# Kernel optimization log

Hardware: AMD Instinct MI355X
Metric: run time of the kernel (lower is better)

Reference implementation:

```python
import jax, jax.numpy as jnp
import numpy as np

N_NODES = 50000
N_EDGES = 300000
D_IN = 256
D_HID = 256


def setup_inputs() -> dict:
    key = jax.random.key(0)
    ks = jax.random.split(key, 9)
    x = jax.random.normal(ks[0], (N_NODES, D_IN), dtype=jnp.float32)
    src = jax.random.randint(ks[1], (N_EDGES,), 0, N_NODES, dtype=jnp.int64)
    dst = jax.random.randint(ks[2], (N_EDGES,), 0, N_NODES, dtype=jnp.int64)
    # Kaiming-uniform-ish init like nn.Linear defaults
    def lin(k, fan_in, fan_out):
        bound = 1.0 / np.sqrt(fan_in)
        kw, kb = jax.random.split(k)
        W = jax.random.uniform(kw, (fan_out, fan_in), minval=-bound, maxval=bound, dtype=jnp.float32)
        b = jax.random.uniform(kb, (fan_out,), minval=-bound, maxval=bound, dtype=jnp.float32)
        return W, b
    W1, b1 = lin(ks[3], 2 * D_IN, D_HID)
    W2, b2 = lin(ks[4], D_HID, D_HID)
    W3, b3 = lin(ks[5], D_HID, 1)
    return {"x": x, "src": src, "dst": dst,
            "W1": W1, "b1": b1, "W2": W2, "b2": b2, "W3": W3, "b3": b3}


def reference(x, src, dst, W1, b1, W2, b2, W3, b3):
    # gather src/dst node features per edge and concat -> [E, 2*D_IN]
    h = jnp.concatenate([x[src], x[dst]], axis=1)
    h = jax.nn.relu(h @ W1.T + b1)          # [E, D_HID]
    h = jax.nn.relu(h @ W2.T + b2)          # dropout is identity in eval mode
    score = h @ W3.T + b3                   # [E, 1]
    return score
```

## Files before the change

kernel.cpp:

```cpp
#include <hip/hip_runtime.h>

typedef short bfx8 __attribute__((ext_vector_type(8)));
typedef short bfx4 __attribute__((ext_vector_type(4)));
typedef float fx4 __attribute__((ext_vector_type(4)));

#define E_TILE 64

__device__ __forceinline__ short f2b(float f) {
  union { float f; unsigned u; } v; v.f = f;
  unsigned u = v.u;
  u += 0x7fffu + ((u >> 16) & 1u);
  return (short)(u >> 16);
}
__device__ __forceinline__ float relu(float f) { return f > 0.f ? f : 0.f; }
__device__ __forceinline__ float asf(unsigned u) { union { unsigned u; float f; } v; v.u = u; return v.f; }
__device__ __forceinline__ unsigned asu(float f) { union { float f; unsigned u; } v; v.f = f; return v.u; }

__global__ void k_prep(const float* __restrict__ W1, const float* __restrict__ W2,
                       unsigned short* __restrict__ B1, unsigned short* __restrict__ W2b) {
  int t = blockIdx.x * 256 + threadIdx.x;
  if (t < 512 * 256) {
    int n = t >> 8, k = t & 255;
    float v = (n < 256) ? W1[n * 512 + k] : W1[(n - 256) * 512 + 256 + k];
    B1[t] = (unsigned short)f2b(v);
  } else if (t < 512 * 256 + 256 * 256) {
    int i = t - 512 * 256;
    W2b[i] = (unsigned short)f2b(W2[i]);
  }
}

__launch_bounds__(512, 4)
__global__ void k_node(const float* __restrict__ x, const unsigned short* __restrict__ B1,
                       const float* __restrict__ b1,
                       unsigned short* __restrict__ PQ, int n_nodes) {
  __shared__ __align__(16) short smA[64 * 40];
  __shared__ __align__(16) short smW[512 * 40];
  short* smT = smW;
  const int tid = threadIdx.x;
  const int wave = tid >> 6, lane = tid & 63;
  const int lr = lane & 15, lg = lane >> 4;
  const int m0 = blockIdx.x * 64;

  fx4 acc[4][4] = {};

#pragma unroll 1
  for (int ks = 0; ks < 8; ++ks) {
    const int k0 = ks * 32;
    {
      int r = tid >> 3, c = (tid & 7) * 4;
      int m = m0 + r;
      bfx4 o;
      if (m < n_nodes) {
        float4 v = *(const float4*)(x + (size_t)m * 256 + k0 + c);
        o[0] = f2b(v.x); o[1] = f2b(v.y); o[2] = f2b(v.z); o[3] = f2b(v.w);
      } else {
        o = (bfx4){0, 0, 0, 0};
      }
      *(bfx4*)&smA[r * 40 + c] = o;
    }
#pragma unroll
    for (int it = 0; it < 4; ++it) {
      int idx = it * 512 + tid;
      int n = idx >> 2, c = (idx & 3) * 8;
      *(bfx8*)&smW[n * 40 + c] = *(const bfx8*)(B1 + n * 256 + k0 + c);
    }
    __syncthreads();
    bfx8 af[4];
#pragma unroll
    for (int mt = 0; mt < 4; ++mt)
      af[mt] = *(const bfx8*)&smA[(mt * 16 + lr) * 40 + lg * 8];
#pragma unroll
    for (int nt = 0; nt < 4; ++nt) {
      bfx8 bf = *(const bfx8*)&smW[(wave * 64 + nt * 16 + lr) * 40 + lg * 8];
#pragma unroll
      for (int mt = 0; mt < 4; ++mt)
        acc[mt][nt] = __builtin_amdgcn_mfma_f32_16x16x32_bf16(af[mt], bf, acc[mt][nt], 0, 0, 0);
    }
    __syncthreads();
  }

  float bias[4];
#pragma unroll
  for (int nt = 0; nt < 4; ++nt) {
    int n = wave * 64 + nt * 16 + lr;
    bias[nt] = (n >= 256) ? b1[n - 256] : 0.f;
  }

#pragma unroll
  for (int h = 0; h < 2; ++h) {
#pragma unroll
    for (int mt2 = 0; mt2 < 2; ++mt2) {
      const int mt = 2 * h + mt2;
#pragma unroll
      for (int nt = 0; nt < 4; ++nt)
#pragma unroll
        for (int i = 0; i < 4; ++i) {
          int mrow = mt2 * 16 + lg * 4 + i;
          int n = wave * 64 + nt * 16 + lr;
          smT[mrow * 520 + n] = f2b(acc[mt][nt][i] + bias[nt]);
        }
    }
    __syncthreads();
    int r = tid >> 4, cbase = (tid & 15) * 8;
    int m = m0 + h * 32 + r;
    if (m < n_nodes) {
#pragma unroll
      for (int j = 0; j < 4; ++j) {
        int c = cbase + j * 128;
        *(bfx8*)(PQ + (size_t)m * 512 + c) = *(const bfx8*)&smT[r * 520 + c];
      }
    }
    __syncthreads();
  }
}

__launch_bounds__(512, 4)
__global__ void k_edge(const unsigned short* __restrict__ PQ,
                       const int* __restrict__ src, const int* __restrict__ dst,
                       const unsigned short* __restrict__ W2b,
                       const float* __restrict__ b2, const float* __restrict__ W3,
                       const float* __restrict__ b3, float* __restrict__ out,
                       int E, int ntiles) {
  __shared__ __align__(16) short smH[64 * 264];
  __shared__ float smS[8][64];
  const int tid = threadIdx.x;
  const int wave = tid >> 6, lane = tid & 63;
  const int lr = lane & 15, lg = lane >> 4;

  bfx8 bw[2][8];
  float b2v[2], w3v[2];
#pragma unroll
  for (int nt = 0; nt < 2; ++nt) {
    int n = wave * 32 + nt * 16 + lr;
    b2v[nt] = b2[n];
    w3v[nt] = W3[n];
#pragma unroll
    for (int ks = 0; ks < 8; ++ks)
      bw[nt][ks] = *(const bfx8*)(W2b + n * 256 + ks * 32 + lg * 8);
  }
  const float b3v = b3[0];

  const int r = tid >> 3;
  const int stride = gridDim.x * E_TILE;

  int e0 = blockIdx.x * E_TILE + r;
  int s_cur = 0, d_cur = 0;
  if (e0 < E) { s_cur = src[e0]; d_cur = dst[e0]; }

  for (int tile = blockIdx.x; tile < ntiles; tile += gridDim.x) {
    const int base = tile * E_TILE;
    const int e = base + r;
    if (e < E) {
      const unsigned* ps = (const unsigned*)(PQ + (size_t)s_cur * 512);
      const unsigned* pd = (const unsigned*)(PQ + (size_t)d_cur * 512 + 256);
#pragma unroll
      for (int it = 0; it < 4; ++it) {
        int c = (tid & 7) * 8 + it * 64;
        uint4 pv = *(const uint4*)(ps + (c >> 1));
        uint4 qv = *(const uint4*)(pd + (c >> 1));
        unsigned o[4];
        const unsigned* pw = (const unsigned*)&pv;
        const unsigned* qw = (const unsigned*)&qv;
#pragma unroll
        for (int w = 0; w < 4; ++w) {
          unsigned up = pw[w], uq = qw[w];
          float slo = relu(asf(up << 16) + asf(uq << 16));
          float shi = relu(asf(up & 0xffff0000u) + asf(uq & 0xffff0000u));
          o[w] = __builtin_amdgcn_perm(asu(shi) + 0x8000u, asu(slo) + 0x8000u,
                                       0x07060302u);
        }
        *(uint4*)&smH[r * 264 + c] = make_uint4(o[0], o[1], o[2], o[3]);
      }
    } else {
#pragma unroll
      for (int it = 0; it < 4; ++it) {
        int c = (tid & 7) * 8 + it * 64;
        *(uint4*)&smH[r * 264 + c] = make_uint4(0, 0, 0, 0);
      }
    }
    int e_next = e + stride;
    if (e_next < E) { s_cur = src[e_next]; d_cur = dst[e_next]; }
    __syncthreads();

    fx4 acc[4][2] = {};
#pragma unroll
    for (int ks = 0; ks < 8; ++ks) {
      bfx8 af[4];
#pragma unroll
      for (int mt = 0; mt < 4; ++mt)
        af[mt] = *(const bfx8*)&smH[(mt * 16 + lr) * 264 + ks * 32 + lg * 8];
#pragma unroll
      for (int nt = 0; nt < 2; ++nt)
#pragma unroll
        for (int mt = 0; mt < 4; ++mt)
          acc[mt][nt] = __builtin_amdgcn_mfma_f32_16x16x32_bf16(af[mt], bw[nt][ks], acc[mt][nt], 0, 0, 0);
    }

#pragma unroll
    for (int mt = 0; mt < 4; ++mt)
#pragma unroll
      for (int i = 0; i < 4; ++i) {
        float p = 0.f;
#pragma unroll
        for (int nt = 0; nt < 2; ++nt)
          p += relu(acc[mt][nt][i] + b2v[nt]) * w3v[nt];
        p += __shfl_xor(p, 1);
        p += __shfl_xor(p, 2);
        p += __shfl_xor(p, 4);
        p += __shfl_xor(p, 8);
        if (lr == 0) smS[wave][mt * 16 + lg * 4 + i] = p;
      }
    __syncthreads();
    if (tid < 64) {
      int eo = base + tid;
      if (eo < E)
        out[eo] = smS[0][tid] + smS[1][tid] + smS[2][tid] + smS[3][tid] +
                  smS[4][tid] + smS[5][tid] + smS[6][tid] + smS[7][tid] + b3v;
    }
    __syncthreads();
  }
}

__global__ void k_fallback(const float* __restrict__ x, const int* __restrict__ src,
                           const int* __restrict__ dst, const float* __restrict__ W1,
                           const float* __restrict__ b1, const float* __restrict__ W2,
                           const float* __restrict__ b2, const float* __restrict__ W3,
                           const float* __restrict__ b3, float* __restrict__ out, int E) {
  __shared__ float smF[4][512];
  __shared__ float smG[4][256];
  int wave = threadIdx.x >> 6, lane = threadIdx.x & 63;
  int e = blockIdx.x * 4 + wave;
  bool valid = e < E;
  int ec = valid ? e : 0;
  int s = src[ec], d = dst[ec];
  for (int j = 0; j < 8; ++j) {
    int k = lane * 8 + j;
    smF[wave][k] = (k < 256) ? x[(size_t)s * 256 + k] : x[(size_t)d * 256 + k - 256];
  }
  __syncthreads();
  for (int t = 0; t < 4; ++t) {
    int n = lane + t * 64;
    float a = b1[n];
    for (int k = 0; k < 512; ++k) a += smF[wave][k] * W1[n * 512 + k];
    smG[wave][n] = relu(a);
  }
  __syncthreads();
  float p = 0.f;
  for (int t = 0; t < 4; ++t) {
    int n = lane + t * 64;
    float a = b2[n];
    for (int k = 0; k < 256; ++k) a += smG[wave][k] * W2[n * 256 + k];
    p += relu(a) * W3[n];
  }
  for (int m = 1; m < 64; m <<= 1) p += __shfl_xor(p, m);
  if (lane == 0 && valid) out[e] = p + b3[0];
}

extern "C" void kernel_launch(void* const* d_in, const int* in_sizes, int n_in,
                              void* d_out, int out_size, void* d_ws, size_t ws_size,
                              hipStream_t stream) {
  const float* x  = (const float*)d_in[0];
  const int*   src = (const int*)d_in[1];
  const int*   dst = (const int*)d_in[2];
  const float* W1 = (const float*)d_in[3];
  const float* b1 = (const float*)d_in[4];
  const float* W2 = (const float*)d_in[5];
  const float* b2 = (const float*)d_in[6];
  const float* W3 = (const float*)d_in[7];
  const float* b3 = (const float*)d_in[8];
  float* out = (float*)d_out;

  const int E = in_sizes[1];
  const int n_nodes = in_sizes[0] / 256;

  const size_t offB1 = 0;
  const size_t offW2 = (size_t)512 * 256 * 2;
  const size_t offPQ = offW2 + (size_t)256 * 256 * 2;
  const size_t need = offPQ + (size_t)n_nodes * 512 * 2;

  if (ws_size >= need) {
    unsigned short* B1  = (unsigned short*)((char*)d_ws + offB1);
    unsigned short* W2b = (unsigned short*)((char*)d_ws + offW2);
    unsigned short* PQ  = (unsigned short*)((char*)d_ws + offPQ);
    k_prep<<<768, 256, 0, stream>>>(W1, W2, B1, W2b);
    k_node<<<(n_nodes + 63) / 64, 512, 0, stream>>>(x, B1, b1, PQ, n_nodes);
    const int ntiles = (E + E_TILE - 1) / E_TILE;
    int grid = ntiles < 512 ? ntiles : 512;
    k_edge<<<grid, 512, 0, stream>>>(PQ, src, dst, W2b, b2, W3, b3, out, E, ntiles);
  } else {
    k_fallback<<<(E + 3) / 4, 256, 0, stream>>>(x, src, dst, W1, b1, W2, b2, W3, b3, out, E);
  }
}
```

Measured before the change: 235.6 us.

## Drop LDS staging in node GEMM, pre-convert x to bf16, widen edge blocks

A new pass converts x to bf16 ahead of time. The node GEMM then loads MFMA operands straight from global memory, which removes the shared-memory staging and its barriers inside the k-loop. The edge kernel moves to 1024-thread blocks of 128 edges, with each wave owning 16 output columns, and launches a grid of 256 blocks. The extra conversion pass costs additional global traffic and a launch. Uncoalesced direct global loads and lower occupancy at 1024 threads could offset the savings.

```diff
diff --git a/kernel.cpp b/kernel.cpp
--- a/kernel.cpp
+++ b/kernel.cpp
@@ -1,10 +1,9 @@
 #include <hip/hip_runtime.h>
 
 typedef short bfx8 __attribute__((ext_vector_type(8)));
-typedef short bfx4 __attribute__((ext_vector_type(4)));
 typedef float fx4 __attribute__((ext_vector_type(4)));
 
-#define E_TILE 64
+#define E_TILE 128
 
 __device__ __forceinline__ short f2b(float f) {
   union { float f; unsigned u; } v; v.f = f;
@@ -29,60 +28,70 @@
   }
 }
 
+__global__ __launch_bounds__(256) void k_convert(const float* __restrict__ x,
+                                                 unsigned short* __restrict__ xb, int n) {
+  int i = (blockIdx.x * 256 + threadIdx.x) * 8;
+  if (i < n) {
+    float4 a = *(const float4*)(x + i);
+    float4 b = *(const float4*)(x + i + 4);
+    bfx8 o;
+    o[0] = f2b(a.x); o[1] = f2b(a.y); o[2] = f2b(a.z); o[3] = f2b(a.w);
+    o[4] = f2b(b.x); o[5] = f2b(b.y); o[6] = f2b(b.z); o[7] = f2b(b.w);
+    *(bfx8*)(xb + i) = o;
+  }
+}
+
+template <bool USE_XB>
 __launch_bounds__(512, 4)
-__global__ void k_node(const float* __restrict__ x, const unsigned short* __restrict__ B1,
-                       const float* __restrict__ b1,
+__global__ void k_node(const float* __restrict__ x, const unsigned short* __restrict__ xb,
+                       const unsigned short* __restrict__ B1, const float* __restrict__ b1,
                        unsigned short* __restrict__ PQ, int n_nodes) {
-  __shared__ __align__(16) short smA[64 * 40];
-  __shared__ __align__(16) short smW[512 * 40];
-  short* smT = smW;
+  __shared__ __align__(16) short smT[32 * 520];
   const int tid = threadIdx.x;
   const int wave = tid >> 6, lane = tid & 63;
   const int lr = lane & 15, lg = lane >> 4;
   const int m0 = blockIdx.x * 64;
+  const int n0 = wave * 64;
+
+  int mrow[4];
+#pragma unroll
+  for (int mt = 0; mt < 4; ++mt) {
+    int m = m0 + mt * 16 + lr;
+    mrow[mt] = m < n_nodes ? m : (n_nodes - 1);
+  }
 
   fx4 acc[4][4] = {};
 
-#pragma unroll 1
+#pragma unroll 2
   for (int ks = 0; ks < 8; ++ks) {
-    const int k0 = ks * 32;
-    {
-      int r = tid >> 3, c = (tid & 7) * 4;
-      int m = m0 + r;
-      bfx4 o;
-      if (m < n_nodes) {
-        float4 v = *(const float4*)(x + (size_t)m * 256 + k0 + c);
-        o[0] = f2b(v.x); o[1] = f2b(v.y); o[2] = f2b(v.z); o[3] = f2b(v.w);
+    bfx8 af[4];
+#pragma unroll
+    for (int mt = 0; mt < 4; ++mt) {
+      if (USE_XB) {
+        af[mt] = *(const bfx8*)(xb + (size_t)mrow[mt] * 256 + ks * 32 + lg * 8);
       } else {
-        o = (bfx4){0, 0, 0, 0};
-      }
-      *(bfx4*)&smA[r * 40 + c] = o;
-    }
-#pragma unroll
-    for (int it = 0; it < 4; ++it) {
-      int idx = it * 512 + tid;
-      int n = idx >> 2, c = (idx & 3) * 8;
-      *(bfx8*)&smW[n * 40 + c] = *(const bfx8*)(B1 + n * 256 + k0 + c);
-    }
-    __syncthreads();
-    bfx8 af[4];
-#pragma unroll
-    for (int mt = 0; mt < 4; ++mt)
-      af[mt] = *(const bfx8*)&smA[(mt * 16 + lr) * 40 + lg * 8];
+        const float* p = x + (size_t)mrow[mt] * 256 + ks * 32 + lg * 8;
+        float4 v0 = *(const float4*)(p);
+        float4 v1 = *(const float4*)(p + 4);
+        bfx8 o;
+        o[0] = f2b(v0.x); o[1] = f2b(v0.y); o[2] = f2b(v0.z); o[3] = f2b(v0.w);
+        o[4] = f2b(v1.x); o[5] = f2b(v1.y); o[6] = f2b(v1.z); o[7] = f2b(v1.w);
+        af[mt] = o;
+      }
+    }
 #pragma unroll
     for (int nt = 0; nt < 4; ++nt) {
-      bfx8 bf = *(const bfx8*)&smW[(wave * 64 + nt * 16 + lr) * 40 + lg * 8];
+      bfx8 bf = *(const bfx8*)(B1 + (size_t)(n0 + nt * 16 + lr) * 256 + ks * 32 + lg * 8);
 #pragma unroll
       for (int mt = 0; mt < 4; ++mt)
         acc[mt][nt] = __builtin_amdgcn_mfma_f32_16x16x32_bf16(af[mt], bf, acc[mt][nt], 0, 0, 0);
     }
-    __syncthreads();
   }
 
   float bias[4];
 #pragma unroll
   for (int nt = 0; nt < 4; ++nt) {
-    int n = wave * 64 + nt * 16 + lr;
+    int n = n0 + nt * 16 + lr;
     bias[nt] = (n >= 256) ? b1[n - 256] : 0.f;
   }
 
@@ -95,9 +104,9 @@
       for (int nt = 0; nt < 4; ++nt)
 #pragma unroll
         for (int i = 0; i < 4; ++i) {
-          int mrow = mt2 * 16 + lg * 4 + i;
-          int n = wave * 64 + nt * 16 + lr;
-          smT[mrow * 520 + n] = f2b(acc[mt][nt][i] + bias[nt]);
+          int mr = mt2 * 16 + lg * 4 + i;
+          int n = n0 + nt * 16 + lr;
+          smT[mr * 520 + n] = f2b(acc[mt][nt][i] + bias[nt]);
         }
     }
     __syncthreads();
@@ -114,33 +123,33 @@
   }
 }
 
-__launch_bounds__(512, 4)
+__launch_bounds__(1024, 4)
 __global__ void k_edge(const unsigned short* __restrict__ PQ,
                        const int* __restrict__ src, const int* __restrict__ dst,
                        const unsigned short* __restrict__ W2b,
                        const float* __restrict__ b2, const float* __restrict__ W3,
                        const float* __restrict__ b3, float* __restrict__ out,
                        int E, int ntiles) {
-  __shared__ __align__(16) short smH[64 * 264];
-  __shared__ float smS[8][64];
+  __shared__ __align__(16) short smH[E_TILE * 264];
+  __shared__ float smS[16][E_TILE];
   const int tid = threadIdx.x;
   const int wave = tid >> 6, lane = tid & 63;
   const int lr = lane & 15, lg = lane >> 4;
 
-  bfx8 bw[2][8];
-  float b2v[2], w3v[2];
-#pragma unroll
-  for (int nt = 0; nt < 2; ++nt) {
-    int n = wave * 32 + nt * 16 + lr;
-    b2v[nt] = b2[n];
-    w3v[nt] = W3[n];
+  bfx8 bw[8];
+  float b2v, w3v;
+  {
+    int n = wave * 16 + lr;
+    b2v = b2[n];
+    w3v = W3[n];
 #pragma unroll
     for (int ks = 0; ks < 8; ++ks)
-      bw[nt][ks] = *(const bfx8*)(W2b + n * 256 + ks * 32 + lg * 8);
+      bw[ks] = *(const bfx8*)(W2b + (size_t)n * 256 + ks * 32 + lg * 8);
   }
   const float b3v = b3[0];
 
   const int r = tid >> 3;
+  const int sub = tid & 7;
   const int stride = gridDim.x * E_TILE;
 
   int e0 = blockIdx.x * E_TILE + r;
@@ -155,7 +164,7 @@
       const unsigned* pd = (const unsigned*)(PQ + (size_t)d_cur * 512 + 256);
 #pragma unroll
       for (int it = 0; it < 4; ++it) {
-        int c = (tid & 7) * 8 + it * 64;
+        int c = sub * 8 + it * 64;
         uint4 pv = *(const uint4*)(ps + (c >> 1));
         uint4 qv = *(const uint4*)(pd + (c >> 1));
         unsigned o[4];
@@ -174,7 +183,7 @@
     } else {
 #pragma unroll
       for (int it = 0; it < 4; ++it) {
-        int c = (tid & 7) * 8 + it * 64;
+        int c = sub * 8 + it * 64;
         *(uint4*)&smH[r * 264 + c] = make_uint4(0, 0, 0, 0);
       }
     }
@@ -182,28 +191,23 @@
     if (e_next < E) { s_cur = src[e_next]; d_cur = dst[e_next]; }
     __syncthreads();
 
-    fx4 acc[4][2] = {};
-#pragma unroll
+    fx4 acc[8];
+#pragma unroll
+    for (int mt = 0; mt < 8; ++mt) acc[mt] = (fx4){0.f, 0.f, 0.f, 0.f};
+#pragma unroll 1
     for (int ks = 0; ks < 8; ++ks) {
-      bfx8 af[4];
-#pragma unroll
-      for (int mt = 0; mt < 4; ++mt)
-        af[mt] = *(const bfx8*)&smH[(mt * 16 + lr) * 264 + ks * 32 + lg * 8];
-#pragma unroll
-      for (int nt = 0; nt < 2; ++nt)
-#pragma unroll
-        for (int mt = 0; mt < 4; ++mt)
-          acc[mt][nt] = __builtin_amdgcn_mfma_f32_16x16x32_bf16(af[mt], bw[nt][ks], acc[mt][nt], 0, 0, 0);
-    }
-
-#pragma unroll
-    for (int mt = 0; mt < 4; ++mt)
+#pragma unroll
+      for (int mt = 0; mt < 8; ++mt) {
+        bfx8 af = *(const bfx8*)&smH[(mt * 16 + lr) * 264 + ks * 32 + lg * 8];
+        acc[mt] = __builtin_amdgcn_mfma_f32_16x16x32_bf16(af, bw[ks], acc[mt], 0, 0, 0);
+      }
+    }
+
+#pragma unroll
+    for (int mt = 0; mt < 8; ++mt)
 #pragma unroll
       for (int i = 0; i < 4; ++i) {
-        float p = 0.f;
-#pragma unroll
-        for (int nt = 0; nt < 2; ++nt)
-          p += relu(acc[mt][nt][i] + b2v[nt]) * w3v[nt];
+        float p = relu(acc[mt][i] + b2v) * w3v;
         p += __shfl_xor(p, 1);
         p += __shfl_xor(p, 2);
         p += __shfl_xor(p, 4);
@@ -211,11 +215,14 @@
         if (lr == 0) smS[wave][mt * 16 + lg * 4 + i] = p;
       }
     __syncthreads();
-    if (tid < 64) {
+    if (tid < E_TILE) {
       int eo = base + tid;
-      if (eo < E)
-        out[eo] = smS[0][tid] + smS[1][tid] + smS[2][tid] + smS[3][tid] +
-                  smS[4][tid] + smS[5][tid] + smS[6][tid] + smS[7][tid] + b3v;
+      if (eo < E) {
+        float s = b3v;
+#pragma unroll
+        for (int w = 0; w < 16; ++w) s += smS[w][tid];
+        out[eo] = s;
+      }
     }
     __syncthreads();
   }
@@ -272,21 +279,35 @@
 
   const int E = in_sizes[1];
   const int n_nodes = in_sizes[0] / 256;
+  const int n_x = in_sizes[0];
 
   const size_t offB1 = 0;
   const size_t offW2 = (size_t)512 * 256 * 2;
-  const size_t offPQ = offW2 + (size_t)256 * 256 * 2;
-  const size_t need = offPQ + (size_t)n_nodes * 512 * 2;
-
-  if (ws_size >= need) {
+  const size_t offXB = offW2 + (size_t)256 * 256 * 2;
+  const size_t offPQ = offXB + (size_t)n_x * 2;
+  const size_t need_full = offPQ + (size_t)n_nodes * 512 * 2;
+  const size_t offPQ2 = offXB;
+  const size_t need_noxb = offPQ2 + (size_t)n_nodes * 512 * 2;
+
+  const int ntiles = (E + E_TILE - 1) / E_TILE;
+  const int egrid = ntiles < 256 ? ntiles : 256;
+
+  if (ws_size >= need_full) {
     unsigned short* B1  = (unsigned short*)((char*)d_ws + offB1);
     unsigned short* W2b = (unsigned short*)((char*)d_ws + offW2);
+    unsigned short* xb  = (unsigned short*)((char*)d_ws + offXB);
     unsigned short* PQ  = (unsigned short*)((char*)d_ws + offPQ);
     k_prep<<<768, 256, 0, stream>>>(W1, W2, B1, W2b);
-    k_node<<<(n_nodes + 63) / 64, 512, 0, stream>>>(x, B1, b1, PQ, n_nodes);
-    const int ntiles = (E + E_TILE - 1) / E_TILE;
-    int grid = ntiles < 512 ? ntiles : 512;
-    k_edge<<<grid, 512, 0, stream>>>(PQ, src, dst, W2b, b2, W3, b3, out, E, ntiles);
+    k_convert<<<(n_x + 2047) / 2048, 256, 0, stream>>>(x, xb, n_x);
+    k_node<true><<<(n_nodes + 63) / 64, 512, 0, stream>>>(x, xb, B1, b1, PQ, n_nodes);
+    k_edge<<<egrid, 1024, 0, stream>>>(PQ, src, dst, W2b, b2, W3, b3, out, E, ntiles);
+  } else if (ws_size >= need_noxb) {
+    unsigned short* B1  = (unsigned short*)((char*)d_ws + offB1);
+    unsigned short* W2b = (unsigned short*)((char*)d_ws + offW2);
+    unsigned short* PQ  = (unsigned short*)((char*)d_ws + offPQ2);
+    k_prep<<<768, 256, 0, stream>>>(W1, W2, B1, W2b);
+    k_node<false><<<(n_nodes + 63) / 64, 512, 0, stream>>>(x, nullptr, B1, b1, PQ, n_nodes);
+    k_edge<<<egrid, 1024, 0, stream>>>(PQ, src, dst, W2b, b2, W3, b3, out, E, ntiles);
   } else {
     k_fallback<<<(E + 3) / 4, 256, 0, stream>>>(x, src, dst, W1, b1, W2, b2, W3, b3, out, E);
   }
```

Result: slower. 857.5 us (+263.9%).
